# Kernel tuning notes

Measured on AMD Instinct MI355X. Metric: run time of the kernel, lower is better.

Reference implementation:

```python
import jax, jax.numpy as jnp
import numpy as np

B, T, DIM, HEADS = 8, 2048, 1024, 16
HD = DIM // HEADS


def setup_inputs() -> dict:
    key = jax.random.key(0)
    ks = jax.random.split(key, 12)
    s = 0.02
    z = jnp.zeros((DIM,), jnp.float32)
    return {
        "x": jax.random.normal(ks[0], (B, T, DIM), jnp.float32),
        "Wq": jax.random.normal(ks[1], (DIM, DIM), jnp.float32) * s,
        "bq": z,
        "Wk": jax.random.normal(ks[2], (DIM, DIM), jnp.float32) * s,
        "bk": z,
        "Wv": jax.random.normal(ks[3], (DIM, DIM), jnp.float32) * s,
        "bv": z,
        "w_rwkv": jax.random.normal(ks[4], (HEADS, HD), jnp.float32) * 0.5,
        "u_rwkv": jax.random.normal(ks[5], (HEADS, HD), jnp.float32) * 0.5,
        "Wo": jax.random.normal(ks[6], (DIM, DIM), jnp.float32) * s,
        "bo": z,
    }


def reference(x, Wq, bq, Wk, bk, Wv, bv, w_rwkv, u_rwkv, Wo, bo):
    N, T_, _ = x.shape
    # queries are computed but never used in the original forward
    _ = x @ Wq + bq
    k = (x @ Wk + bk).reshape(N, T_, HEADS, HD)
    v = (x @ Wv + bv).reshape(N, T_, HEADS, HD)
    kt = jnp.moveaxis(k, 1, 0)  # [T, N, H, D]
    vt = jnp.moveaxis(v, 1, 0)  # [T, N, H, D]

    u = u_rwkv  # [H, D] broadcasts against [N, H, D]
    w = w_rwkv

    def step(carry, kv):
        pp, aa, bb = carry
        k_t, v_t = kv
        # output at step t (with bonus u)
        ww = u + k_t
        qq = jnp.maximum(ww, pp)
        e1 = jnp.exp(pp - qq)
        e2 = jnp.exp(ww - qq)
        o_t = (e1 * aa + e2 * v_t) / (e1 * bb + e2)
        # state update (with decay w)
        ww2 = pp - w
        qq2 = jnp.maximum(ww2, k_t)
        e1b = jnp.exp(ww2 - qq2)
        e2b = jnp.exp(k_t - qq2)
        aa2 = e1b * aa + e2b * v_t
        bb2 = e1b * bb + e2b
        return (qq2, aa2, bb2), o_t

    init = (kt[0], vt[0], jnp.ones_like(kt[0]))  # pp, aa, bb
    _, o_rest = jax.lax.scan(step, init, (kt[1:], vt[1:]))  # [T-1, N, H, D]
    O = jnp.concatenate([vt[:1], o_rest], axis=0)  # O[0] = v[0]
    O = jnp.moveaxis(O, 0, 1).reshape(N, T_, -1)  # [N, T, dim]
    return O @ Wo + bo
```

## Files before the change

kernel.cpp:

```cpp
#include <hip/hip_runtime.h>

#define DIMSZ 1024
#define NB 8
#define TSEQ 2048
#define MTOT (NB*TSEQ)
#define CCH 64
#define LCH (TSEQ/CCH)
#define NCHAN (NB*DIMSZ)

typedef __attribute__((ext_vector_type(8))) short short8v;
typedef __attribute__((ext_vector_type(4))) float f32x4;

__device__ __forceinline__ unsigned short f2bf(float f) {
  unsigned int u; __builtin_memcpy(&u, &f, 4);
  unsigned int r = u + 0x7FFF + ((u >> 16) & 1);
  return (unsigned short)(r >> 16);
}
__device__ __forceinline__ float bf2f(unsigned short us) {
  unsigned int v = ((unsigned int)us) << 16;
  float f; __builtin_memcpy(&f, &v, 4); return f;
}

__device__ __forceinline__ void gload16(const void* g, void* l) {
  __builtin_amdgcn_global_load_lds(
      (const __attribute__((address_space(1))) void*)g,
      (__attribute__((address_space(3))) void*)l, 16, 0, 0);
}

__global__ __launch_bounds__(256) void cast_x_kernel(
    const float* __restrict__ in, unsigned short* __restrict__ out) {
  int i = blockIdx.x * 256 + threadIdx.x;
  float4 f = reinterpret_cast<const float4*>(in)[i];
  uint2 o;
  o.x = (unsigned)f2bf(f.x) | ((unsigned)f2bf(f.y) << 16);
  o.y = (unsigned)f2bf(f.z) | ((unsigned)f2bf(f.w) << 16);
  reinterpret_cast<uint2*>(out)[i] = o;
}

__global__ __launch_bounds__(256) void transpose_cast_kernel(
    const float* __restrict__ W, unsigned short* __restrict__ WT) {
  __shared__ float tile[32][33];
  int tx = threadIdx.x & 31, ty = threadIdx.x >> 5;
  int row0 = blockIdx.y * 32, col0 = blockIdx.x * 32;
  #pragma unroll
  for (int j = 0; j < 32; j += 8)
    tile[ty + j][tx] = W[(size_t)(row0 + ty + j) * DIMSZ + col0 + tx];
  __syncthreads();
  #pragma unroll
  for (int j = 0; j < 32; j += 8)
    WT[(size_t)(col0 + ty + j) * DIMSZ + row0 + tx] = f2bf(tile[tx][ty + j]);
}


#define VM2 asm volatile("s_waitcnt vmcnt(2)" ::: "memory")
#define VM0 asm volatile("s_waitcnt vmcnt(0)" ::: "memory")

#define PH_BAR do {                         \
  __builtin_amdgcn_s_barrier();             \
  __builtin_amdgcn_sched_barrier(0);        \
} while(0)

#define STAGE(BUF, OP, HALF, T) do {                                        \
  const unsigned short* _s = (OP) ? BT : Aop;                               \
  const int _rb = ((OP) ? bcol : brow) + (HALF)*128 + wid*16;               \
  char* _lb = smem + (OP)*65536 + (BUF)*32768 + (HALF)*16384 + wid*2048;    \
  const size_t _k0 = (size_t)(T)*64;                                        \
  gload16(&_s[(size_t)(_rb + srow)*K + _k0 + (sg^srow)*8], _lb);            \
  gload16(&_s[(size_t)(_rb + 8 + srow)*K + _k0 + (sg^srow)*8], _lb + 1024); \
} while(0)

#define RD16(P, OFF) (*(const short8v*)((P) + (OFF)))

#define READ_A(DST, BUF, MH) do {                                           \
  _Pragma("unroll")                                                         \
  for (int _m = 0; _m < 4; ++_m) {                                          \
    DST[_m][0] = RD16(pA0, (BUF)*32768 + (MH)*16384 + _m*2048);             \
    DST[_m][1] = RD16(pA1, (BUF)*32768 + (MH)*16384 + _m*2048);             \
  }                                                                         \
} while(0)

#define READ_B(DST, BUF, NH) do {                                           \
  _Pragma("unroll")                                                         \
  for (int _n = 0; _n < 2; ++_n) {                                          \
    DST[_n][0] = RD16(pB0, (BUF)*32768 + (NH)*16384 + _n*2048);             \
    DST[_n][1] = RD16(pB1, (BUF)*32768 + (NH)*16384 + _n*2048);             \
  }                                                                         \
} while(0)

#define MFMA_Q(MH, NH, AF, BF) do {                                         \
  __builtin_amdgcn_s_setprio(1);                                            \
  _Pragma("unroll")                                                         \
  for (int _m = 0; _m < 4; ++_m)                                            \
    _Pragma("unroll")                                                       \
    for (int _n = 0; _n < 2; ++_n) {                                        \
      acc[(MH)*4+_m][(NH)*2+_n] = __builtin_amdgcn_mfma_f32_16x16x32_bf16(  \
          AF[_m][0], BF[_n][0], acc[(MH)*4+_m][(NH)*2+_n], 0, 0, 0);        \
      acc[(MH)*4+_m][(NH)*2+_n] = __builtin_amdgcn_mfma_f32_16x16x32_bf16(  \
          AF[_m][1], BF[_n][1], acc[(MH)*4+_m][(NH)*2+_n], 0, 0, 0);        \
    }                                                                       \
  __builtin_amdgcn_s_setprio(0);                                            \
} while(0)

#define TILE(B_, NB_, T) do {                                               \
  const int _t = (T);                                                       \
  const bool s1 = (_t + 1 < NT);                                            \
                                                                   \
  READ_B(bf1, B_, 1);                                                       \
  if (s1) STAGE(NB_, 0, 0, _t + 1);                                         \
  if (s1) { VM2; } else { VM0; }                        \
  PH_BAR;                                                                   \
  MFMA_Q(0, 0, a0, bf0); PH_BAR;                                            \
                                                                   \
  READ_A(a1, B_, 1);                                                        \
  if (s1) STAGE(NB_, 1, 0, _t + 1);                                         \
  PH_BAR;                                                                   \
  MFMA_Q(0, 1, a0, bf1); PH_BAR;                                            \
                                                                   \
  if (s1) STAGE(NB_, 1, 1, _t + 1);                                         \
  PH_BAR;                                                                   \
  MFMA_Q(1, 0, a1, bf0); PH_BAR;                                            \
     \
  if (s1) { STAGE(NB_, 0, 1, _t + 1); VM2; }                                \
  PH_BAR;                                                                   \
  if (s1) { READ_A(a0, NB_, 0); READ_B(bf0, NB_, 0); }                      \
  MFMA_Q(1, 1, a1, bf1); PH_BAR;                                            \
} while(0)

template<int OUTBF>
__global__ __launch_bounds__(512) void gemm256_kernel(
    const unsigned short* __restrict__ Aop,
    const unsigned short* __restrict__ BT,
    void* __restrict__ Cv,
    const float* __restrict__ bias0,
    const float* __restrict__ bias1,
    int M, int N, int K, int Nsplit) {
  extern __shared__ char smem[];
  const int tid  = threadIdx.x;
  const int wid  = tid >> 6;
  const int lane = tid & 63;
  const int wr   = wid >> 2;
  const int wc   = wid & 3;
  const int brow = blockIdx.x * 256;
  const int bcol = blockIdx.y * 256;
  const int lrow = lane & 15;
  const int lko  = (lane >> 4) * 8;
  const int rds  = (lrow & 7) << 4;
  const int srow = lane >> 3;
  const int sg   = lane & 7;

  const char* pA0 = smem + (wr*64 + lrow)*128 + ((lko*2) ^ rds);
  const char* pA1 = smem + (wr*64 + lrow)*128 + ((64 + lko*2) ^ rds);
  const char* pB0 = smem + 65536 + (wc*32 + lrow)*128 + ((lko*2) ^ rds);
  const char* pB1 = smem + 65536 + (wc*32 + lrow)*128 + ((64 + lko*2) ^ rds);

  f32x4 acc[8][4];
  #pragma unroll
  for (int m = 0; m < 8; ++m)
    #pragma unroll
    for (int n = 0; n < 4; ++n)
      acc[m][n] = (f32x4){0.f, 0.f, 0.f, 0.f};

  short8v a0[4][2], a1[4][2], bf0[2][2], bf1[2][2];

  STAGE(0, 0, 0, 0); STAGE(0, 1, 0, 0); STAGE(0, 1, 1, 0); STAGE(0, 0, 1, 0);
  VM2;
  PH_BAR;
  READ_A(a0, 0, 0); READ_B(bf0, 0, 0);

  const int NT = K >> 6;
  for (int t = 0; t < NT; t += 2) {
    TILE(0, 1, t);
    TILE(1, 0, t + 1);
  }

  #pragma unroll
  for (int mf = 0; mf < 8; ++mf) {
    const int rowb = brow + (mf >= 4) * 128 + wr * 64 + (mf & 3) * 16 + (lane >> 4) * 4;
    #pragma unroll
    for (int nf = 0; nf < 4; ++nf) {
      const int col = bcol + (nf >= 2) * 128 + wc * 32 + (nf & 1) * 16 + lrow;
      const float bb = (col < Nsplit) ? bias0[col] : bias1[col - Nsplit];
      #pragma unroll
      for (int r = 0; r < 4; ++r) {
        const float val = acc[mf][nf][r] + bb;
        if (OUTBF) {
          ((unsigned short*)Cv)[(size_t)(rowb + r) * N + col] = f2bf(val);
        } else {
          ((float*)Cv)[(size_t)(rowb + r) * N + col] = val;
        }
      }
    }
  }
}


__device__ __forceinline__ void wkv_step(float& p, float& a, float& b,
                                         float kt, float vt, float w) {
  float ww2 = p - w;
  float qq2 = fmaxf(ww2, kt);
  float e1 = __expf(ww2 - qq2);
  float e2 = __expf(kt - qq2);
  a = e1 * a + e2 * vt;
  b = e1 * b + e2;
  p = qq2;
}

__global__ __launch_bounds__(256) void wkv_chunk_state_kernel(
    const unsigned short* __restrict__ kv,
    const float* __restrict__ wdec,
    float* __restrict__ stP, float* __restrict__ stA, float* __restrict__ stB) {
  int idx = blockIdx.x * 256 + threadIdx.x;
  int cq = idx & 255;
  int n = (idx >> 8) & (NB - 1);
  int chunk = idx >> 11;
  int c = cq * 4;
  float4 w4 = *reinterpret_cast<const float4*>(&wdec[c]);
  const unsigned short* base = kv + (size_t)(n * TSEQ + chunk * LCH) * 2048 + c;
  float p0=-1e30f,a0=0.f,b0=0.f, p1=-1e30f,a1=0.f,b1=0.f;
  float p2=-1e30f,a2=0.f,b2=0.f, p3=-1e30f,a3=0.f,b3=0.f;
  #pragma unroll 8
  for (int j = 0; j < LCH; ++j) {
    uint2 kk = *reinterpret_cast<const uint2*>(&base[(size_t)j * 2048]);
    uint2 vv = *reinterpret_cast<const uint2*>(&base[(size_t)j * 2048 + 1024]);
    wkv_step(p0,a0,b0, bf2f(kk.x & 0xffff), bf2f(vv.x & 0xffff), w4.x);
    wkv_step(p1,a1,b1, bf2f(kk.x >> 16),    bf2f(vv.x >> 16),    w4.y);
    wkv_step(p2,a2,b2, bf2f(kk.y & 0xffff), bf2f(vv.y & 0xffff), w4.z);
    wkv_step(p3,a3,b3, bf2f(kk.y >> 16),    bf2f(vv.y >> 16),    w4.w);
  }
  int soff = chunk * NCHAN + n * 1024 + c;
  *reinterpret_cast<float4*>(&stP[soff]) = make_float4(p0, p1, p2, p3);
  *reinterpret_cast<float4*>(&stA[soff]) = make_float4(a0, a1, a2, a3);
  *reinterpret_cast<float4*>(&stB[soff]) = make_float4(b0, b1, b2, b3);
}

__global__ __launch_bounds__(256) void wkv_scan_kernel(
    const float* __restrict__ wdec,
    float* __restrict__ stP, float* __restrict__ stA, float* __restrict__ stB) {
  int idx = blockIdx.x * 256 + threadIdx.x;
  int c = idx & 1023;
  float decay = (float)LCH * wdec[c];
  float p = -1e30f, a = 0.f, b = 0.f;
  for (int i = 0; i < CCH; ++i) {
    int off = i * NCHAN + idx;
    float pc = stP[off], ac = stA[off], bc = stB[off];
    stP[off] = p; stA[off] = a; stB[off] = b;
    float pd = p - decay;
    float q = fmaxf(pd, pc);
    float e1 = __expf(pd - q);
    float e2 = __expf(pc - q);
    a = e1 * a + e2 * ac;
    b = e1 * b + e2 * bc;
    p = q;
  }
}

__global__ __launch_bounds__(256) void wkv_out_kernel(
    const unsigned short* __restrict__ kv,
    const float* __restrict__ wdec, const float* __restrict__ ubon,
    const float* __restrict__ stP, const float* __restrict__ stA,
    const float* __restrict__ stB,
    unsigned short* __restrict__ O) {
  int idx = blockIdx.x * 256 + threadIdx.x;
  int cq = idx & 255;
  int n = (idx >> 8) & (NB - 1);
  int chunk = idx >> 11;
  int c = cq * 4;
  float4 w4 = *reinterpret_cast<const float4*>(&wdec[c]);
  float4 u4 = *reinterpret_cast<const float4*>(&ubon[c]);
  const unsigned short* base = kv + (size_t)(n * TSEQ + chunk * LCH) * 2048 + c;
  unsigned short* ob = O + (size_t)(n * TSEQ + chunk * LCH) * DIMSZ + c;
  int soff = chunk * NCHAN + n * 1024 + c;
  float4 pP = *reinterpret_cast<const float4*>(&stP[soff]);
  float4 pA = *reinterpret_cast<const float4*>(&stA[soff]);
  float4 pB = *reinterpret_cast<const float4*>(&stB[soff]);
  float p0=pP.x,a0=pA.x,b0=pB.x, p1=pP.y,a1=pA.y,b1=pB.y;
  float p2=pP.z,a2=pA.z,b2=pB.z, p3=pP.w,a3=pA.w,b3=pB.w;
  #pragma unroll 4
  for (int j = 0; j < LCH; ++j) {
    uint2 kk = *reinterpret_cast<const uint2*>(&base[(size_t)j * 2048]);
    uint2 vv = *reinterpret_cast<const uint2*>(&base[(size_t)j * 2048 + 1024]);
    float k0 = bf2f(kk.x & 0xffff), k1 = bf2f(kk.x >> 16);
    float k2 = bf2f(kk.y & 0xffff), k3 = bf2f(kk.y >> 16);
    float v0 = bf2f(vv.x & 0xffff), v1 = bf2f(vv.x >> 16);
    float v2 = bf2f(vv.y & 0xffff), v3 = bf2f(vv.y >> 16);
    float ww0=u4.x+k0, ww1=u4.y+k1, ww2=u4.z+k2, ww3=u4.w+k3;
    float qq0=fmaxf(ww0,p0), qq1=fmaxf(ww1,p1), qq2=fmaxf(ww2,p2), qq3=fmaxf(ww3,p3);
    float e10=__expf(p0-qq0), e20=__expf(ww0-qq0);
    float e11=__expf(p1-qq1), e21=__expf(ww1-qq1);
    float e12=__expf(p2-qq2), e22=__expf(ww2-qq2);
    float e13=__expf(p3-qq3), e23=__expf(ww3-qq3);
    float o0=(e10*a0+e20*v0)*__builtin_amdgcn_rcpf(e10*b0+e20);
    float o1=(e11*a1+e21*v1)*__builtin_amdgcn_rcpf(e11*b1+e21);
    float o2=(e12*a2+e22*v2)*__builtin_amdgcn_rcpf(e12*b2+e22);
    float o3=(e13*a3+e23*v3)*__builtin_amdgcn_rcpf(e13*b3+e23);
    uint2 ow;
    ow.x = (unsigned)f2bf(o0) | ((unsigned)f2bf(o1) << 16);
    ow.y = (unsigned)f2bf(o2) | ((unsigned)f2bf(o3) << 16);
    *reinterpret_cast<uint2*>(&ob[(size_t)j * DIMSZ]) = ow;
    wkv_step(p0,a0,b0,k0,v0,w4.x);
    wkv_step(p1,a1,b1,k1,v1,w4.y);
    wkv_step(p2,a2,b2,k2,v2,w4.z);
    wkv_step(p3,a3,b3,k3,v3,w4.w);
  }
}

extern "C" void kernel_launch(void* const* d_in, const int* in_sizes, int n_in,
                              void* d_out, int out_size, void* d_ws, size_t ws_size,
                              hipStream_t stream) {
  const float* x  = (const float*)d_in[0];
  const float* Wk = (const float*)d_in[3];
  const float* bk = (const float*)d_in[4];
  const float* Wv = (const float*)d_in[5];
  const float* bv = (const float*)d_in[6];
  const float* wr = (const float*)d_in[7];
  const float* ur = (const float*)d_in[8];
  const float* Wo = (const float*)d_in[9];
  const float* bo = (const float*)d_in[10];
  float* out = (float*)d_out;

  char* ws = (char*)d_ws;
  unsigned short* xb   = (unsigned short*)(ws);
  unsigned short* WTkv = (unsigned short*)(ws + 33554432);
  unsigned short* WoT  = (unsigned short*)(ws + 37748736);
  unsigned short* kvb  = (unsigned short*)(ws + 39845888);

  float* stP = out;
  float* stA = out + CCH * NCHAN;
  float* stB = out + 2 * CCH * NCHAN;

  cast_x_kernel<<<dim3(16384), dim3(256), 0, stream>>>(x, xb);
  transpose_cast_kernel<<<dim3(32, 32), dim3(256), 0, stream>>>(Wk, WTkv);
  transpose_cast_kernel<<<dim3(32, 32), dim3(256), 0, stream>>>(Wv, WTkv + 1024 * 1024);
  transpose_cast_kernel<<<dim3(32, 32), dim3(256), 0, stream>>>(Wo, WoT);

  gemm256_kernel<1><<<dim3(64, 8), dim3(512), 131072, stream>>>(
      xb, WTkv, (void*)kvb, bk, bv, MTOT, 2048, 1024, 1024);

  wkv_chunk_state_kernel<<<dim3(CCH * NB), dim3(256), 0, stream>>>(
      kvb, wr, stP, stA, stB);
  wkv_scan_kernel<<<dim3(NCHAN / 256), dim3(256), 0, stream>>>(wr, stP, stA, stB);
  wkv_out_kernel<<<dim3(CCH * NB), dim3(256), 0, stream>>>(
      kvb, wr, ur, stP, stA, stB, xb);

  gemm256_kernel<0><<<dim3(64, 4), dim3(512), 131072, stream>>>(
      xb, WoT, (void*)out, bo, bo, MTOT, 1024, 1024, 1024);
}
```

Baseline: 175.1 us.

## Restructure GEMM LDS layout and pipeline; merge weight transpose launches

Changes the shared-memory layout so each buffer holds contiguous A and B halves, and replaces the two-tile unrolled TILE schedule with a single-tile loop plus an epilogue using different vmcnt waits and read placement. It also fuses the three weight transpose-cast launches into one 3D-grid launch to cut launch overhead. The new pipeline reads fragments after the barrier instead of prefetching them in the previous tile, which may expose more LDS latency. The vmcnt counts must also match the outstanding loads exactly, or correctness is at risk.

```diff
diff --git a/kernel.cpp b/kernel.cpp
--- a/kernel.cpp
+++ b/kernel.cpp
@@ -37,8 +37,13 @@
   reinterpret_cast<uint2*>(out)[i] = o;
 }
 
-__global__ __launch_bounds__(256) void transpose_cast_kernel(
-    const float* __restrict__ W, unsigned short* __restrict__ WT) {
+__global__ __launch_bounds__(256) void transpose_cast3_kernel(
+    const float* __restrict__ Wk, const float* __restrict__ Wv,
+    const float* __restrict__ Wo,
+    unsigned short* __restrict__ WTk, unsigned short* __restrict__ WTv,
+    unsigned short* __restrict__ WTo) {
+  const float* W = (blockIdx.z == 0) ? Wk : (blockIdx.z == 1) ? Wv : Wo;
+  unsigned short* WT = (blockIdx.z == 0) ? WTk : (blockIdx.z == 1) ? WTv : WTo;
   __shared__ float tile[32][33];
   int tx = threadIdx.x & 31, ty = threadIdx.x >> 5;
   int row0 = blockIdx.y * 32, col0 = blockIdx.x * 32;
@@ -52,6 +57,7 @@
 }
 
 
+#define VM4 asm volatile("s_waitcnt vmcnt(4)" ::: "memory")
 #define VM2 asm volatile("s_waitcnt vmcnt(2)" ::: "memory")
 #define VM0 asm volatile("s_waitcnt vmcnt(0)" ::: "memory")
 
@@ -63,27 +69,29 @@
 #define STAGE(BUF, OP, HALF, T) do {                                        \
   const unsigned short* _s = (OP) ? BT : Aop;                               \
   const int _rb = ((OP) ? bcol : brow) + (HALF)*128 + wid*16;               \
-  char* _lb = smem + (OP)*65536 + (BUF)*32768 + (HALF)*16384 + wid*2048;    \
+  char* _lb = smem + (BUF)*65536 + (OP)*32768 + ((HALF)*128 + wid*16)*128;  \
   const size_t _k0 = (size_t)(T)*64;                                        \
   gload16(&_s[(size_t)(_rb + srow)*K + _k0 + (sg^srow)*8], _lb);            \
   gload16(&_s[(size_t)(_rb + 8 + srow)*K + _k0 + (sg^srow)*8], _lb + 1024); \
 } while(0)
 
-#define RD16(P, OFF) (*(const short8v*)((P) + (OFF)))
-
 #define READ_A(DST, BUF, MH) do {                                           \
   _Pragma("unroll")                                                         \
   for (int _m = 0; _m < 4; ++_m) {                                          \
-    DST[_m][0] = RD16(pA0, (BUF)*32768 + (MH)*16384 + _m*2048);             \
-    DST[_m][1] = RD16(pA1, (BUF)*32768 + (MH)*16384 + _m*2048);             \
+    const char* _pa = smem + (BUF)*65536 +                                  \
+        ((MH)*128 + wr*64 + _m*16 + lrow)*128;                              \
+    DST[_m][0] = *(const short8v*)(_pa + ((lko*2) ^ rds));                  \
+    DST[_m][1] = *(const short8v*)(_pa + (((32+lko)*2) ^ rds));             \
   }                                                                         \
 } while(0)
 
 #define READ_B(DST, BUF, NH) do {                                           \
   _Pragma("unroll")                                                         \
   for (int _n = 0; _n < 2; ++_n) {                                          \
-    DST[_n][0] = RD16(pB0, (BUF)*32768 + (NH)*16384 + _n*2048);             \
-    DST[_n][1] = RD16(pB1, (BUF)*32768 + (NH)*16384 + _n*2048);             \
+    const char* _pb = smem + (BUF)*65536 + 32768 +                          \
+        ((NH)*128 + wc*32 + _n*16 + lrow)*128;                              \
+    DST[_n][0] = *(const short8v*)(_pb + ((lko*2) ^ rds));                  \
+    DST[_n][1] = *(const short8v*)(_pb + (((32+lko)*2) ^ rds));             \
   }                                                                         \
 } while(0)
 
@@ -99,31 +107,7 @@
           AF[_m][1], BF[_n][1], acc[(MH)*4+_m][(NH)*2+_n], 0, 0, 0);        \
     }                                                                       \
   __builtin_amdgcn_s_setprio(0);                                            \
-} while(0)
-
-#define TILE(B_, NB_, T) do {                                               \
-  const int _t = (T);                                                       \
-  const bool s1 = (_t + 1 < NT);                                            \
-                                                                   \
-  READ_B(bf1, B_, 1);                                                       \
-  if (s1) STAGE(NB_, 0, 0, _t + 1);                                         \
-  if (s1) { VM2; } else { VM0; }                        \
   PH_BAR;                                                                   \
-  MFMA_Q(0, 0, a0, bf0); PH_BAR;                                            \
-                                                                   \
-  READ_A(a1, B_, 1);                                                        \
-  if (s1) STAGE(NB_, 1, 0, _t + 1);                                         \
-  PH_BAR;                                                                   \
-  MFMA_Q(0, 1, a0, bf1); PH_BAR;                                            \
-                                                                   \
-  if (s1) STAGE(NB_, 1, 1, _t + 1);                                         \
-  PH_BAR;                                                                   \
-  MFMA_Q(1, 0, a1, bf0); PH_BAR;                                            \
-     \
-  if (s1) { STAGE(NB_, 0, 1, _t + 1); VM2; }                                \
-  PH_BAR;                                                                   \
-  if (s1) { READ_A(a0, NB_, 0); READ_B(bf0, NB_, 0); }                      \
-  MFMA_Q(1, 1, a1, bf1); PH_BAR;                                            \
 } while(0)
 
 template<int OUTBF>
@@ -148,11 +132,6 @@
   const int srow = lane >> 3;
   const int sg   = lane & 7;
 
-  const char* pA0 = smem + (wr*64 + lrow)*128 + ((lko*2) ^ rds);
-  const char* pA1 = smem + (wr*64 + lrow)*128 + ((64 + lko*2) ^ rds);
-  const char* pB0 = smem + 65536 + (wc*32 + lrow)*128 + ((lko*2) ^ rds);
-  const char* pB1 = smem + 65536 + (wc*32 + lrow)*128 + ((64 + lko*2) ^ rds);
-
   f32x4 acc[8][4];
   #pragma unroll
   for (int m = 0; m < 8; ++m)
@@ -162,15 +141,41 @@
 
   short8v a0[4][2], a1[4][2], bf0[2][2], bf1[2][2];
 
-  STAGE(0, 0, 0, 0); STAGE(0, 1, 0, 0); STAGE(0, 1, 1, 0); STAGE(0, 0, 1, 0);
-  VM2;
+  STAGE(0, 0, 0, 0);
+  STAGE(0, 1, 0, 0);
+  STAGE(0, 1, 1, 0);
+  STAGE(0, 0, 1, 0);
+  VM4;
   PH_BAR;
-  READ_A(a0, 0, 0); READ_B(bf0, 0, 0);
 
   const int NT = K >> 6;
-  for (int t = 0; t < NT; t += 2) {
-    TILE(0, 1, t);
-    TILE(1, 0, t + 1);
+  for (int t = 0; t < NT - 1; ++t) {
+    const int b = t & 1, nb = b ^ 1;
+    READ_A(a0, b, 0); READ_B(bf0, b, 0);
+    STAGE(nb, 0, 0, t + 1); VM4; PH_BAR;
+    MFMA_Q(0, 0, a0, bf0);
+    READ_B(bf1, b, 1);
+    STAGE(nb, 1, 0, t + 1); VM4; PH_BAR;
+    MFMA_Q(0, 1, a0, bf1);
+    READ_A(a1, b, 1);
+    STAGE(nb, 1, 1, t + 1); PH_BAR;
+    MFMA_Q(1, 0, a1, bf0);
+    STAGE(nb, 0, 1, t + 1); VM4; PH_BAR;
+    MFMA_Q(1, 1, a1, bf1);
+  }
+  {
+    const int b = (NT - 1) & 1;
+    READ_A(a0, b, 0); READ_B(bf0, b, 0);
+    VM2; PH_BAR;
+    MFMA_Q(0, 0, a0, bf0);
+    READ_B(bf1, b, 1);
+    VM0; PH_BAR;
+    MFMA_Q(0, 1, a0, bf1);
+    READ_A(a1, b, 1);
+    PH_BAR;
+    MFMA_Q(1, 0, a1, bf0);
+    PH_BAR;
+    MFMA_Q(1, 1, a1, bf1);
   }
 
   #pragma unroll
@@ -329,9 +334,8 @@
   float* stB = out + 2 * CCH * NCHAN;
 
   cast_x_kernel<<<dim3(16384), dim3(256), 0, stream>>>(x, xb);
-  transpose_cast_kernel<<<dim3(32, 32), dim3(256), 0, stream>>>(Wk, WTkv);
-  transpose_cast_kernel<<<dim3(32, 32), dim3(256), 0, stream>>>(Wv, WTkv + 1024 * 1024);
-  transpose_cast_kernel<<<dim3(32, 32), dim3(256), 0, stream>>>(Wo, WoT);
+  transpose_cast3_kernel<<<dim3(32, 32, 3), dim3(256), 0, stream>>>(
+      Wk, Wv, Wo, WTkv, WTkv + 1024 * 1024, WoT);
 
   gemm256_kernel<1><<<dim3(64, 8), dim3(512), 131072, stream>>>(
       xb, WTkv, (void*)kvb, bk, bv, MTOT, 2048, 1024, 1024);
```

Result: faster. 167.5 us, median of 2 (-4.4%).
